# Kernel optimization log

Measured on AMD Instinct MI355X. Metric: run time of the kernel, lower is better.

Reference implementation:

```python
import jax, jax.numpy as jnp
import numpy as np

# config constants
B, S, H = 4, 2048, 1024
E = 8                 # n_routed_experts
M = 512               # moe_intermediate_size
K = 2                 # num_experts_per_tok
N_SHARED = 2
SM = M * N_SHARED     # shared expert intermediate
G = 64                # gene_size
GE_TEMP = 1.0
ALPHA = 0.001         # aux_loss_alpha
SEQ_AUX = True
NORM_TOPK = True
COS_TEMP = 0.78
CONS_ALPHA = 0.01
LEAKY_SLOPE = 0.01
EPS_COS = 1e-8


def setup_inputs() -> dict:
    key = jax.random.key(0)
    ks = jax.random.split(key, 12)
    sh = 1.0 / np.sqrt(H)
    sm = 1.0 / np.sqrt(M)
    ssm = 1.0 / np.sqrt(SM)
    sg = 1.0 / np.sqrt(G)
    return {
        "hidden_states": jax.random.normal(ks[0], (B, S, H), jnp.float32),
        "g": jax.random.normal(ks[1], (B, G), jnp.float32),
        "wt": jax.random.uniform(ks[2], (E, H), jnp.float32, -sh, sh),   # gate weight_token
        "wg": jax.random.uniform(ks[3], (E, G), jnp.float32, -sg, sg),   # gate weight_gene
        "w_gate": jax.random.uniform(ks[4], (E, H, M), jnp.float32, -sh, sh),
        "w_up": jax.random.uniform(ks[5], (E, H, M), jnp.float32, -sh, sh),
        "w_down": jax.random.uniform(ks[6], (E, M, H), jnp.float32, -sm, sm),
        "sw_gate": jax.random.uniform(ks[7], (H, SM), jnp.float32, -sh, sh),
        "sw_up": jax.random.uniform(ks[8], (H, SM), jnp.float32, -sh, sh),
        "sw_down": jax.random.uniform(ks[9], (SM, H), jnp.float32, -ssm, ssm),
    }


def _leaky(x):
    return jnp.where(x >= 0, x, LEAKY_SLOPE * x)


def _moe_forward(hidden_states, g, wt, wg, w_gate, w_up, w_down, sw_gate, sw_up, sw_down):
    b, s, h = hidden_states.shape
    x = hidden_states.reshape(-1, h)                    # [T, H], T = b*s
    T = x.shape[0]

    # ---- gate ----
    logits_h = x @ wt.T                                 # [T, E]
    logits_g = g @ wg.T                                 # [b, E]
    logits_g = jnp.repeat(logits_g, s, axis=0)          # [T, E]
    logits = (logits_h + logits_g / GE_TEMP) / (1.0 + 1.0 / GE_TEMP)
    scores = jax.nn.softmax(logits, axis=-1)            # [T, E]
    topk_w, topk_idx = jax.lax.top_k(scores, K)         # [T, K]
    if K > 1 and NORM_TOPK:
        topk_w = topk_w / (topk_w.sum(-1, keepdims=True) + 1e-20)

    # aux loss (seq_aux=True)
    onehot = jax.nn.one_hot(topk_idx.reshape(b, s * K), E, dtype=jnp.float32)  # [b, s*K, E]
    ce = onehot.sum(1) / (s * K / E)                    # [b, E]
    aux_loss = (ce * scores.reshape(b, s, E).mean(1)).sum(1).mean() * ALPHA

    # ---- routed experts: dense stacked compute, then gather ----
    gp = _leaky(jnp.einsum('th,ehm->etm', x, w_gate))   # [E, T, M]
    up = jnp.einsum('th,ehm->etm', x, w_up)
    y_all = jnp.einsum('etm,emh->eth', gp * up, w_down) # [E, T, H]
    y_sel = y_all[topk_idx, jnp.arange(T)[:, None], :]  # [T, K, H]
    y = (y_sel * topk_w[..., None]).sum(1).reshape(b, s, h)

    # ---- shared expert ----
    p = (_leaky(hidden_states @ sw_gate) * (hidden_states @ sw_up)) @ sw_down
    y = y + p

    # consistency cosine loss
    num = jnp.sum(y * p, -1)
    den = jnp.maximum(jnp.linalg.norm(y, axis=-1), EPS_COS) * jnp.maximum(jnp.linalg.norm(p, axis=-1), EPS_COS)
    closs = CONS_ALPHA * jnp.mean((num / den) / (1.0 + COS_TEMP))
    return y, aux_loss + closs


def reference(hidden_states, g, wt, wg, w_gate, w_up, w_down, sw_gate, sw_up, sw_down):
    y, _ = _moe_forward(hidden_states, g, wt, wg, w_gate, w_up, w_down, sw_gate, sw_up, sw_down)
    return y
```

## Files before the change

kernel.cpp:

```cpp
#include <hip/hip_runtime.h>
#include <stdint.h>

#define T_TOK 8192
#define H_DIM 1024
#define M_DIM 512
#define SM_DIM 1024
#define E_NUM 8
#define S_SEQ 2048
#define G_DIM 64
#define NASSIGN 16384
#define NSLOT (NASSIGN + E_NUM * 256)
#define MAX_TILES (NASSIGN / 256 + E_NUM)
#define NBLK_PLACE (NASSIGN / 256)

typedef float f32x4 __attribute__((ext_vector_type(4)));
typedef short bf16x8 __attribute__((ext_vector_type(8)));

struct TileDesc { int base; int expert; int nrows; };

#define WAITCNT_VM6 asm volatile("s_waitcnt vmcnt(6)" ::: "memory")
#define WAITCNT_VM4 asm volatile("s_waitcnt vmcnt(4)" ::: "memory")
#define WAITCNT_VM2 asm volatile("s_waitcnt vmcnt(2)" ::: "memory")
#define WAITCNT_VM0 asm volatile("s_waitcnt vmcnt(0)" ::: "memory")
#define WAITCNT_LGKM0 asm volatile("s_waitcnt lgkmcnt(0)" ::: "memory")

static __device__ __forceinline__ ushort f2b(float f) {
  union { float f; uint32_t u; } a; a.f = f;
  uint32_t r = a.u + 0x7fffu + ((a.u >> 16) & 1u);
  return (ushort)(r >> 16);
}
static __device__ __forceinline__ float b2f(ushort u) {
  union { uint32_t u; float f; } a; a.u = ((uint32_t)u) << 16;
  return a.f;
}
static __device__ __forceinline__ int imin(int a, int b) { return a < b ? a : b; }

static __device__ __forceinline__ void gll16(const void* g, void* l) {
  __builtin_amdgcn_global_load_lds(
      (const __attribute__((address_space(1))) void*)g,
      (__attribute__((address_space(3))) void*)l, 16, 0, 0);
}
static __device__ __forceinline__ int xcd_remap(int wg, int nwg) {
  return (wg & 7) * (nwg >> 3) + (wg >> 3);
}

__global__ __launch_bounds__(256) void prep_kernel(
    const float* __restrict__ x, const float* __restrict__ wt, const float* __restrict__ g,
    const float* __restrict__ wgm,
    const float* __restrict__ w_gate, const float* __restrict__ w_up,
    const float* __restrict__ w_down, const float* __restrict__ sw_gate,
    const float* __restrict__ sw_up, const float* __restrict__ sw_down,
    ushort* __restrict__ wg_t, ushort* __restrict__ wu_t,
    ushort* __restrict__ wd_t, ushort* __restrict__ swg_t,
    ushort* __restrict__ swu_t, ushort* __restrict__ swd_t,
    ushort* __restrict__ xb, int* __restrict__ tidx, float* __restrict__ tw) {
  __shared__ float tile[32][33];
  int id = blockIdx.x;
  if (id < 15360) {
    int tx = threadIdx.x & 31, ty = threadIdx.x >> 5;
    const float* src; ushort* dst; int R, C, t;
    if (id < 4096)        { src = w_gate;  dst = wg_t;  R = 1024; C = 512;  t = id; }
    else if (id < 8192)   { src = w_up;    dst = wu_t;  R = 1024; C = 512;  t = id - 4096; }
    else if (id < 12288)  { src = w_down;  dst = wd_t;  R = 512;  C = 1024; t = id - 8192; }
    else if (id < 13312)  { src = sw_gate; dst = swg_t; R = 1024; C = 1024; t = id - 12288; }
    else if (id < 14336)  { src = sw_up;   dst = swu_t; R = 1024; C = 1024; t = id - 13312; }
    else                  { src = sw_down; dst = swd_t; R = 1024; C = 1024; t = id - 14336; }
    int tc = C >> 5;
    int tpm = (R >> 5) * tc;
    int e = t / tpm, tt = t % tpm;
    int c0 = (tt % tc) * 32, r0 = (tt / tc) * 32;
    size_t bo = (size_t)e * R * C;
    src += bo; dst += bo;
#pragma unroll
    for (int i = 0; i < 4; ++i)
      tile[ty + i * 8][tx] = src[(size_t)(r0 + ty + i * 8) * C + c0 + tx];
    __syncthreads();
#pragma unroll
    for (int i = 0; i < 4; ++i)
      dst[(size_t)(c0 + ty + i * 8) * R + r0 + tx] = f2b(tile[tx][ty + i * 8]);
    return;
  }
  int id2 = id - 15360;
  int wv = threadIdx.x >> 6, lane = threadIdx.x & 63;
  int t = id2 * 4 + wv;
  const float4* xr4 = (const float4*)x + (size_t)t * 256;
  ushort4* xb4 = (ushort4*)xb + (size_t)t * 256;
  float a[E_NUM];
#pragma unroll
  for (int e = 0; e < E_NUM; ++e) a[e] = 0.f;
#pragma unroll
  for (int j = 0; j < 4; ++j) {
    float4 v = xr4[lane + 64 * j];
    ushort4 o;
    o.x = f2b(v.x); o.y = f2b(v.y); o.z = f2b(v.z); o.w = f2b(v.w);
    xb4[lane + 64 * j] = o;
#pragma unroll
    for (int e = 0; e < E_NUM; ++e) {
      float4 wv4 = ((const float4*)(wt + (size_t)e * H_DIM))[lane + 64 * j];
      a[e] += v.x * wv4.x + v.y * wv4.y + v.z * wv4.z + v.w * wv4.w;
    }
  }
#pragma unroll
  for (int e = 0; e < E_NUM; ++e)
    for (int off = 32; off; off >>= 1) a[e] += __shfl_xor(a[e], off, 64);
  float lge = 0.f;
  int b = t / S_SEQ;
  if (lane < E_NUM) {
    const float* gv = g + b * G_DIM;
    const float* wv2 = wgm + lane * G_DIM;
    for (int i = 0; i < G_DIM; ++i) lge += gv[i] * wv2[i];
  }
  float l[E_NUM];
#pragma unroll
  for (int e = 0; e < E_NUM; ++e) l[e] = 0.5f * (a[e] + __shfl(lge, e, 64));
  if (lane == 0) {
    int i1 = 0; float b1 = l[0];
#pragma unroll
    for (int e = 1; e < E_NUM; ++e) if (l[e] > b1) { b1 = l[e]; i1 = e; }
    int i2 = -1; float b2 = -1e30f;
#pragma unroll
    for (int e = 0; e < E_NUM; ++e) if (e != i1 && l[e] > b2) { b2 = l[e]; i2 = e; }
    float e2 = expf(b2 - b1);
    float inv = 1.f / (1.f + e2);
    tidx[t * 2] = i1; tidx[t * 2 + 1] = i2;
    tw[t * 2] = inv;  tw[t * 2 + 1] = e2 * inv;
  }
}

__global__ __launch_bounds__(256) void hist_kernel(const int* __restrict__ tidx,
                                                   int* __restrict__ bcount) {
  __shared__ int h[E_NUM];
  int tid = threadIdx.x;
  if (tid < E_NUM) h[tid] = 0;
  __syncthreads();
  atomicAdd(&h[tidx[blockIdx.x * 256 + tid]], 1);
  __syncthreads();
  if (tid < E_NUM) bcount[blockIdx.x * E_NUM + tid] = h[tid];
}

__global__ __launch_bounds__(64) void scan2_kernel(
    const int* __restrict__ bcount, int* __restrict__ boffs, int* __restrict__ offs,
    TileDesc* __restrict__ desc, int* __restrict__ ndesc) {
  __shared__ int cnt[E_NUM];
  __shared__ int off_s[E_NUM];
  int lane = threadIdx.x;
  if (lane < E_NUM) {
    int s = 0;
    for (int b = 0; b < NBLK_PLACE; ++b) s += bcount[b * E_NUM + lane];
    cnt[lane] = s;
  }
  __syncthreads();
  if (lane == 0) {
    int o = 0, nd = 0;
    for (int e = 0; e < E_NUM; ++e) {
      off_s[e] = o;
      offs[e] = o;
      int n = cnt[e];
      for (int tb = 0; tb < n; tb += 256) {
        desc[nd].base = o + tb; desc[nd].expert = e;
        desc[nd].nrows = imin(n - tb, 256);
        ++nd;
      }
      o += n;
    }
    offs[E_NUM] = o;
    *ndesc = nd;
  }
  __syncthreads();
  if (lane < E_NUM) {
    int run = off_s[lane];
    for (int b = 0; b < NBLK_PLACE; ++b) {
      boffs[b * E_NUM + lane] = run;
      run += bcount[b * E_NUM + lane];
    }
  }
}

__global__ __launch_bounds__(256) void place2_kernel(
    const int* __restrict__ tidx, const int* __restrict__ boffs,
    int* __restrict__ perm, int* __restrict__ slot_of) {
  __shared__ int wcnt[4][E_NUM];
  int tid = threadIdx.x, wv = tid >> 6, lane = tid & 63;
  int i = blockIdx.x * 256 + tid;
  int e = tidx[i];
  unsigned long long lower = (lane == 63) ? 0x7fffffffffffffffull : ((1ull << lane) - 1ull);
  int rank = 0;
#pragma unroll
  for (int ee = 0; ee < E_NUM; ++ee) {
    unsigned long long m = __ballot(e == ee);
    if (e == ee) rank = __popcll(m & lower);
    if (lane == 0) wcnt[wv][ee] = __popcll(m);
  }
  __syncthreads();
  int off = boffs[blockIdx.x * E_NUM + e];
  for (int w = 0; w < wv; ++w) off += wcnt[w][e];
  int pos = off + rank;
  perm[pos] = i >> 1;
  slot_of[i] = pos;
}

template <int DUAL>
static __device__ __forceinline__ void gemm_core8(
    const ushort* __restrict__ A, const ushort* __restrict__ B0,
    const ushort* __restrict__ B1, void* __restrict__ Out, int outf32,
    int Kd, int NdOut, int rowbase, int nrows, int n0,
    const int* __restrict__ perm, ushort* __restrict__ LDS) {
  int tid = threadIdx.x, wv = tid >> 6, lane = tid & 63;
  int wr = wv >> 2, wc = wv & 3;
  int lr = lane & 15, cg = lane >> 4;
  int sid = lane >> 3, dch = lane & 7;

  const ushort* apA[2][2];
  const ushort* apB[2][2];
#pragma unroll
  for (int qm = 0; qm < 2; ++qm)
#pragma unroll
    for (int k = 0; k < 2; ++k) {
      int idx = k * 64 + wv * 8 + sid;
      int gch = dch ^ (idx & 7);
      int grow = (idx >> 6) * 128 + qm * 64 + (idx & 63);
      grow = imin(grow, nrows - 1);
      int arow = perm ? perm[rowbase + grow] : rowbase + grow;
      apA[qm][k] = A + (size_t)arow * Kd + gch * 8;
    }
#pragma unroll
  for (int qn = 0; qn < 2; ++qn)
#pragma unroll
    for (int k = 0; k < 2; ++k) {
      int idx = k * 64 + wv * 8 + sid;
      int gch = dch ^ (idx & 7);
      int vrow = n0 + (idx >> 5) * 64 + qn * 32 + (idx & 31);
      const ushort* src; int brow;
      if (DUAL) {
        src = ((vrow >> 4) & 1) ? B1 : B0;
        brow = (vrow >> 5) * 16 + (vrow & 15);
      } else {
        src = B0; brow = vrow;
      }
      apB[qn][k] = src + (size_t)brow * Kd + gch * 8;
    }

  auto stgA = [&](int qm, int k, int nd) {
    gll16(apA[qm][k], LDS + nd * 16384 + qm * 8192 + (k * 512 + wv * 64) * 8);
    apA[qm][k] += 64;
  };
  auto stgB = [&](int qn, int k, int nd) {
    gll16(apB[qn][k], LDS + 32768 + nd * 16384 + qn * 8192 + (k * 512 + wv * 64) * 8);
    apB[qn][k] += 64;
  };
  auto rdA = [&](int d, int qm, int m, int kk) -> bf16x8 {
    int idx = wr * 64 + m * 16 + lr;
    int ch = (kk * 4 + cg) ^ (idx & 7);
    return *(const bf16x8*)(LDS + d * 16384 + qm * 8192 + idx * 64 + ch * 8);
  };
  auto rdB = [&](int d, int qn, int n, int kk) -> bf16x8 {
    int idx = wc * 32 + n * 16 + lr;
    int ch = (kk * 4 + cg) ^ (idx & 7);
    return *(const bf16x8*)(LDS + 32768 + d * 16384 + qn * 8192 + idx * 64 + ch * 8);
  };

  f32x4 acc[2][2][4][2];
#pragma unroll
  for (int qm = 0; qm < 2; ++qm)
#pragma unroll
    for (int qn = 0; qn < 2; ++qn)
#pragma unroll
      for (int m = 0; m < 4; ++m)
#pragma unroll
        for (int n = 0; n < 2; ++n) acc[qm][qn][m][n] = (f32x4){0.f, 0.f, 0.f, 0.f};

  int nk = Kd >> 6;
  stgA(0, 0, 0); stgA(0, 1, 0);
  stgB(0, 0, 0); stgB(0, 1, 0);
  stgB(1, 0, 0); stgB(1, 1, 0);
  stgA(1, 0, 0); stgA(1, 1, 0);
  WAITCNT_VM4;
  __builtin_amdgcn_s_barrier();

  for (int t = 0; t < nk; ++t) {
    int cur = t & 1, nxt = cur ^ 1;
    bool hn = (t + 1 < nk);
    bf16x8 a0f[4][2], a1f[4][2], b0f[2][2], b1f[2][2];

#pragma unroll
    for (int m = 0; m < 4; ++m) { a0f[m][0] = rdA(cur, 0, m, 0); a0f[m][1] = rdA(cur, 0, m, 1); }
#pragma unroll
    for (int n = 0; n < 2; ++n) { b0f[n][0] = rdB(cur, 0, n, 0); b0f[n][1] = rdB(cur, 0, n, 1); }
    if (hn) { stgA(0, 0, nxt); stgA(0, 1, nxt); WAITCNT_VM4; } else { WAITCNT_VM2; }
    WAITCNT_LGKM0;
    __builtin_amdgcn_s_barrier();
    __builtin_amdgcn_s_setprio(1);
#pragma unroll
    for (int m = 0; m < 4; ++m)
#pragma unroll
      for (int n = 0; n < 2; ++n) {
        acc[0][0][m][n] = __builtin_amdgcn_mfma_f32_16x16x32_bf16(a0f[m][0], b0f[n][0], acc[0][0][m][n], 0, 0, 0);
        acc[0][0][m][n] = __builtin_amdgcn_mfma_f32_16x16x32_bf16(a0f[m][1], b0f[n][1], acc[0][0][m][n], 0, 0, 0);
      }
    __builtin_amdgcn_s_setprio(0);

#pragma unroll
    for (int n = 0; n < 2; ++n) { b1f[n][0] = rdB(cur, 1, n, 0); b1f[n][1] = rdB(cur, 1, n, 1); }
    if (hn) { stgB(0, 0, nxt); stgB(0, 1, nxt); WAITCNT_VM4; } else { WAITCNT_VM0; }
    WAITCNT_LGKM0;
    __builtin_amdgcn_s_barrier();
    __builtin_amdgcn_s_setprio(1);
#pragma unroll
    for (int m = 0; m < 4; ++m)
#pragma unroll
      for (int n = 0; n < 2; ++n) {
        acc[0][1][m][n] = __builtin_amdgcn_mfma_f32_16x16x32_bf16(a0f[m][0], b1f[n][0], acc[0][1][m][n], 0, 0, 0);
        acc[0][1][m][n] = __builtin_amdgcn_mfma_f32_16x16x32_bf16(a0f[m][1], b1f[n][1], acc[0][1][m][n], 0, 0, 0);
      }
    __builtin_amdgcn_s_setprio(0);

#pragma unroll
    for (int m = 0; m < 4; ++m) { a1f[m][0] = rdA(cur, 1, m, 0); a1f[m][1] = rdA(cur, 1, m, 1); }
    if (hn) { stgB(1, 0, nxt); stgB(1, 1, nxt); WAITCNT_VM6; }
    WAITCNT_LGKM0;
    __builtin_amdgcn_s_barrier();
    __builtin_amdgcn_s_setprio(1);
#pragma unroll
    for (int m = 0; m < 4; ++m)
#pragma unroll
      for (int n = 0; n < 2; ++n) {
        acc[1][0][m][n] = __builtin_amdgcn_mfma_f32_16x16x32_bf16(a1f[m][0], b0f[n][0], acc[1][0][m][n], 0, 0, 0);
        acc[1][0][m][n] = __builtin_amdgcn_mfma_f32_16x16x32_bf16(a1f[m][1], b0f[n][1], acc[1][0][m][n], 0, 0, 0);
      }
    __builtin_amdgcn_s_setprio(0);

    if (hn) { stgA(1, 0, nxt); stgA(1, 1, nxt); WAITCNT_VM4; }
    WAITCNT_LGKM0;
    __builtin_amdgcn_s_barrier();
    __builtin_amdgcn_s_setprio(1);
#pragma unroll
    for (int m = 0; m < 4; ++m)
#pragma unroll
      for (int n = 0; n < 2; ++n) {
        acc[1][1][m][n] = __builtin_amdgcn_mfma_f32_16x16x32_bf16(a1f[m][0], b1f[n][0], acc[1][1][m][n], 0, 0, 0);
        acc[1][1][m][n] = __builtin_amdgcn_mfma_f32_16x16x32_bf16(a1f[m][1], b1f[n][1], acc[1][1][m][n], 0, 0, 0);
      }
    __builtin_amdgcn_s_setprio(0);
  }

#pragma unroll
  for (int qm = 0; qm < 2; ++qm)
#pragma unroll
    for (int qn = 0; qn < 2; ++qn)
#pragma unroll
      for (int m = 0; m < 4; ++m)
#pragma unroll
        for (int r = 0; r < 4; ++r) {
          int row = wr * 128 + qm * 64 + m * 16 + cg * 4 + r;
          if (row < nrows) {
            if (DUAL) {
              float gv = acc[qm][qn][m][0][r], uv = acc[qm][qn][m][1][r];
              float hv = (gv >= 0.f ? gv : 0.01f * gv) * uv;
              int col = ((n0 >> 5) + wc * 2 + qn) * 16 + lr;
              ((ushort*)Out)[(size_t)(rowbase + row) * NdOut + col] = f2b(hv);
            } else {
#pragma unroll
              for (int n = 0; n < 2; ++n) {
                int col = n0 + wc * 64 + qn * 32 + n * 16 + lr;
                size_t o = (size_t)(rowbase + row) * NdOut + col;
                if (outf32) ((float*)Out)[o] = acc[qm][qn][m][n][r];
                else ((ushort*)Out)[o] = f2b(acc[qm][qn][m][n][r]);
              }
            }
          }
        }
}

__global__ __launch_bounds__(512) void gemm_dual_all(
    const ushort* __restrict__ xb, const ushort* __restrict__ swg,
    const ushort* __restrict__ swu, ushort* __restrict__ hsh,
    const ushort* __restrict__ wg, const ushort* __restrict__ wu,
    ushort* __restrict__ h_e, const int* __restrict__ perm,
    const TileDesc* __restrict__ desc, const int* __restrict__ ndesc) {
  __shared__ ushort LDS[65536];
  int id = xcd_remap(blockIdx.x, gridDim.x);
  if (id < 256) {
    int mt = id >> 3, n0 = (id & 7) * 256;
    gemm_core8<1>(xb, swg, swu, hsh, 0, H_DIM, SM_DIM, mt * 256, 256, n0, nullptr, LDS);
  } else {
    int rid = id - 256;
    int mt = rid >> 2, n0 = (rid & 3) * 256;
    if (mt >= *ndesc) return;
    TileDesc d = desc[mt];
    size_t wo = (size_t)d.expert * M_DIM * H_DIM;
    gemm_core8<1>(xb, wg + wo, wu + wo, h_e, 0, H_DIM, M_DIM, d.base, d.nrows, n0, perm, LDS);
  }
}

__global__ __launch_bounds__(512) void gemm_down_all(
    const ushort* __restrict__ hsh, const ushort* __restrict__ swd, ushort* __restrict__ ysh,
    const ushort* __restrict__ h_e, const ushort* __restrict__ wd, ushort* __restrict__ ye,
    const TileDesc* __restrict__ desc, const int* __restrict__ ndesc) {
  __shared__ ushort LDS[65536];
  int id = xcd_remap(blockIdx.x, gridDim.x);
  if (id < 128) {
    int mt = id >> 2, n0 = (id & 3) * 256;
    gemm_core8<0>(hsh, swd, nullptr, (void*)ysh, 0, SM_DIM, H_DIM, mt * 256, 256, n0, nullptr, LDS);
  } else {
    int rid = id - 128;
    int mt = rid >> 2, n0 = (rid & 3) * 256;
    if (mt >= *ndesc) return;
    TileDesc d = desc[mt];
    gemm_core8<0>(h_e, wd + (size_t)d.expert * H_DIM * M_DIM, nullptr, (void*)ye, 0,
                  M_DIM, H_DIM, d.base, d.nrows, n0, nullptr, LDS);
  }
}

__global__ __launch_bounds__(256) void final_kernel(
    float* __restrict__ y, const ushort* __restrict__ ysh, const ushort* __restrict__ ye,
    const int* __restrict__ slot_of, const float* __restrict__ tw) {
  for (int i = blockIdx.x * 256 + threadIdx.x; i < T_TOK * H_DIM / 4; i += 2048 * 256) {
    int t = i >> 8;
    int c4 = (i & 255) * 4;
    int s0 = slot_of[t * 2], s1 = slot_of[t * 2 + 1];
    float w0 = tw[t * 2], w1 = tw[t * 2 + 1];
    ushort4 pp = *(const ushort4*)(ysh + (size_t)t * H_DIM + c4);
    ushort4 a = *(const ushort4*)(ye + (size_t)s0 * H_DIM + c4);
    ushort4 b = *(const ushort4*)(ye + (size_t)s1 * H_DIM + c4);
    float4 v;
    v.x = b2f(pp.x) + w0 * b2f(a.x) + w1 * b2f(b.x);
    v.y = b2f(pp.y) + w0 * b2f(a.y) + w1 * b2f(b.y);
    v.z = b2f(pp.z) + w0 * b2f(a.z) + w1 * b2f(b.z);
    v.w = b2f(pp.w) + w0 * b2f(a.w) + w1 * b2f(b.w);
    ((float4*)y)[i] = v;
  }
}

extern "C" void kernel_launch(void* const* d_in, const int* in_sizes, int n_in,
                              void* d_out, int out_size, void* d_ws, size_t ws_size,
                              hipStream_t stream) {
  const float* x       = (const float*)d_in[0];
  const float* g       = (const float*)d_in[1];
  const float* wt      = (const float*)d_in[2];
  const float* wg      = (const float*)d_in[3];
  const float* w_gate  = (const float*)d_in[4];
  const float* w_up    = (const float*)d_in[5];
  const float* w_down  = (const float*)d_in[6];
  const float* sw_gate = (const float*)d_in[7];
  const float* sw_up   = (const float*)d_in[8];
  const float* sw_down = (const float*)d_in[9];
  float* y = (float*)d_out;

  char* p = (char*)d_ws;
  auto alloc = [&](size_t bytes) -> char* {
    char* r = p;
    p += (bytes + 255) & ~(size_t)255;
    return r;
  };
  ushort* xb    = (ushort*)alloc((size_t)T_TOK * H_DIM * 2);
  ushort* wg_t  = (ushort*)alloc((size_t)E_NUM * M_DIM * H_DIM * 2);
  ushort* wu_t  = (ushort*)alloc((size_t)E_NUM * M_DIM * H_DIM * 2);
  ushort* wd_t  = (ushort*)alloc((size_t)E_NUM * H_DIM * M_DIM * 2);
  ushort* swg_t = (ushort*)alloc((size_t)SM_DIM * H_DIM * 2);
  ushort* swu_t = (ushort*)alloc((size_t)SM_DIM * H_DIM * 2);
  ushort* swd_t = (ushort*)alloc((size_t)H_DIM * SM_DIM * 2);
  int* tidx     = (int*)alloc(NASSIGN * 4);
  float* tw     = (float*)alloc(NASSIGN * 4);
  int* bcount   = (int*)alloc(NBLK_PLACE * E_NUM * 4);
  int* boffs    = (int*)alloc(NBLK_PLACE * E_NUM * 4);
  int* offs     = (int*)alloc((E_NUM + 1) * 4);
  int* ndesc    = (int*)alloc(4);
  int* perm     = (int*)alloc(NASSIGN * 4);
  int* slot_of  = (int*)alloc(NASSIGN * 4);
  TileDesc* desc = (TileDesc*)alloc(MAX_TILES * sizeof(TileDesc));
  ushort* h_e   = (ushort*)alloc((size_t)NSLOT * M_DIM * 2);
  ushort* hsh   = (ushort*)alloc((size_t)T_TOK * SM_DIM * 2);
  ushort* ye    = (ushort*)alloc((size_t)NSLOT * H_DIM * 2);
  ushort* ysh   = (ushort*)alloc((size_t)T_TOK * H_DIM * 2);
  (void)ws_size; (void)in_sizes; (void)n_in; (void)out_size;

  prep_kernel<<<15360 + 2048, 256, 0, stream>>>(
      x, wt, g, wg, w_gate, w_up, w_down, sw_gate, sw_up, sw_down,
      wg_t, wu_t, wd_t, swg_t, swu_t, swd_t, xb, tidx, tw);
  hist_kernel<<<NBLK_PLACE, 256, 0, stream>>>(tidx, bcount);
  scan2_kernel<<<1, 64, 0, stream>>>(bcount, boffs, offs, desc, ndesc);
  place2_kernel<<<NBLK_PLACE, 256, 0, stream>>>(tidx, boffs, perm, slot_of);

  gemm_dual_all<<<256 + MAX_TILES * 4, 512, 0, stream>>>(
      xb, swg_t, swu_t, hsh, wg_t, wu_t, h_e, perm, desc, ndesc);
  gemm_down_all<<<128 + MAX_TILES * 4, 512, 0, stream>>>(
      hsh, swd_t, ysh, h_e, wd_t, ye, desc, ndesc);

  final_kernel<<<2048, 256, 0, stream>>>(y, ysh, ye, slot_of, tw);
}
```

Baseline: 207.5 us.

## Fuse routing histogram and scan into prep and place kernels; drop redundant LDS waits

Per-chunk expert counts are now built with global atomics inside the gate/prep kernel. Each place block computes its own prefix offsets and the tile descriptors directly. This removes the separate histogram and single-block scan kernels and their launch and serialization cost, at the price of a memset, global atomics and a redundant per-block prefix loop. Separately, the GEMM main loop drops explicit lgkmcnt(0) waits before barriers and reorders the B fragment reads ahead of the A reads, leaving the compiler to place LDS waits so more latency can overlap.

New measurement: 212.8 us. +2.5%, slower.

```diff
diff --git a/kernel.cpp b/kernel.cpp
--- a/kernel.cpp
+++ b/kernel.cpp
@@ -22,7 +22,6 @@
 #define WAITCNT_VM4 asm volatile("s_waitcnt vmcnt(4)" ::: "memory")
 #define WAITCNT_VM2 asm volatile("s_waitcnt vmcnt(2)" ::: "memory")
 #define WAITCNT_VM0 asm volatile("s_waitcnt vmcnt(0)" ::: "memory")
-#define WAITCNT_LGKM0 asm volatile("s_waitcnt lgkmcnt(0)" ::: "memory")
 
 static __device__ __forceinline__ ushort f2b(float f) {
   union { float f; uint32_t u; } a; a.f = f;
@@ -53,7 +52,8 @@
     ushort* __restrict__ wg_t, ushort* __restrict__ wu_t,
     ushort* __restrict__ wd_t, ushort* __restrict__ swg_t,
     ushort* __restrict__ swu_t, ushort* __restrict__ swd_t,
-    ushort* __restrict__ xb, int* __restrict__ tidx, float* __restrict__ tw) {
+    ushort* __restrict__ xb, int* __restrict__ tidx, float* __restrict__ tw,
+    int* __restrict__ bcount) {
   __shared__ float tile[32][33];
   int id = blockIdx.x;
   if (id < 15360) {
@@ -124,37 +124,38 @@
     float inv = 1.f / (1.f + e2);
     tidx[t * 2] = i1; tidx[t * 2 + 1] = i2;
     tw[t * 2] = inv;  tw[t * 2 + 1] = e2 * inv;
-  }
-}
-
-__global__ __launch_bounds__(256) void hist_kernel(const int* __restrict__ tidx,
-                                                   int* __restrict__ bcount) {
-  __shared__ int h[E_NUM];
-  int tid = threadIdx.x;
-  if (tid < E_NUM) h[tid] = 0;
-  __syncthreads();
-  atomicAdd(&h[tidx[blockIdx.x * 256 + tid]], 1);
-  __syncthreads();
-  if (tid < E_NUM) bcount[blockIdx.x * E_NUM + tid] = h[tid];
-}
-
-__global__ __launch_bounds__(64) void scan2_kernel(
-    const int* __restrict__ bcount, int* __restrict__ boffs, int* __restrict__ offs,
+    int chunk = t >> 7;
+    atomicAdd(&bcount[chunk * E_NUM + i1], 1);
+    atomicAdd(&bcount[chunk * E_NUM + i2], 1);
+  }
+}
+
+__global__ __launch_bounds__(256) void place2_kernel(
+    const int* __restrict__ tidx, const int* __restrict__ bcount,
+    int* __restrict__ perm, int* __restrict__ slot_of,
     TileDesc* __restrict__ desc, int* __restrict__ ndesc) {
   __shared__ int cnt[E_NUM];
-  __shared__ int off_s[E_NUM];
-  int lane = threadIdx.x;
-  if (lane < E_NUM) {
-    int s = 0;
-    for (int b = 0; b < NBLK_PLACE; ++b) s += bcount[b * E_NUM + lane];
-    cnt[lane] = s;
+  __shared__ int myoff[E_NUM];
+  __shared__ int wcnt[4][E_NUM];
+  int tid = threadIdx.x, wv = tid >> 6, lane = tid & 63, blk = blockIdx.x;
+  if (tid < E_NUM) {
+    int run = 0, mine = 0;
+    for (int b = 0; b < NBLK_PLACE; ++b) {
+      if (b == blk) mine = run;
+      run += bcount[b * E_NUM + tid];
+    }
+    cnt[tid] = run;
+    myoff[tid] = mine;
   }
   __syncthreads();
-  if (lane == 0) {
+  if (tid < E_NUM) {
+    int o = 0;
+    for (int e = 0; e < tid; ++e) o += cnt[e];
+    myoff[tid] += o;
+  }
+  if (blk == 0 && tid == 32) {
     int o = 0, nd = 0;
     for (int e = 0; e < E_NUM; ++e) {
-      off_s[e] = o;
-      offs[e] = o;
       int n = cnt[e];
       for (int tb = 0; tb < n; tb += 256) {
         desc[nd].base = o + tb; desc[nd].expert = e;
@@ -163,25 +164,9 @@
       }
       o += n;
     }
-    offs[E_NUM] = o;
     *ndesc = nd;
   }
-  __syncthreads();
-  if (lane < E_NUM) {
-    int run = off_s[lane];
-    for (int b = 0; b < NBLK_PLACE; ++b) {
-      boffs[b * E_NUM + lane] = run;
-      run += bcount[b * E_NUM + lane];
-    }
-  }
-}
-
-__global__ __launch_bounds__(256) void place2_kernel(
-    const int* __restrict__ tidx, const int* __restrict__ boffs,
-    int* __restrict__ perm, int* __restrict__ slot_of) {
-  __shared__ int wcnt[4][E_NUM];
-  int tid = threadIdx.x, wv = tid >> 6, lane = tid & 63;
-  int i = blockIdx.x * 256 + tid;
+  int i = blk * 256 + tid;
   int e = tidx[i];
   unsigned long long lower = (lane == 63) ? 0x7fffffffffffffffull : ((1ull << lane) - 1ull);
   int rank = 0;
@@ -192,7 +177,7 @@
     if (lane == 0) wcnt[wv][ee] = __popcll(m);
   }
   __syncthreads();
-  int off = boffs[blockIdx.x * E_NUM + e];
+  int off = myoff[e];
   for (int w = 0; w < wv; ++w) off += wcnt[w][e];
   int pos = off + rank;
   perm[pos] = i >> 1;
@@ -283,11 +268,10 @@
     bf16x8 a0f[4][2], a1f[4][2], b0f[2][2], b1f[2][2];
 
 #pragma unroll
+    for (int n = 0; n < 2; ++n) { b0f[n][0] = rdB(cur, 0, n, 0); b0f[n][1] = rdB(cur, 0, n, 1); }
+#pragma unroll
     for (int m = 0; m < 4; ++m) { a0f[m][0] = rdA(cur, 0, m, 0); a0f[m][1] = rdA(cur, 0, m, 1); }
-#pragma unroll
-    for (int n = 0; n < 2; ++n) { b0f[n][0] = rdB(cur, 0, n, 0); b0f[n][1] = rdB(cur, 0, n, 1); }
     if (hn) { stgA(0, 0, nxt); stgA(0, 1, nxt); WAITCNT_VM4; } else { WAITCNT_VM2; }
-    WAITCNT_LGKM0;
     __builtin_amdgcn_s_barrier();
     __builtin_amdgcn_s_setprio(1);
 #pragma unroll
@@ -302,7 +286,6 @@
 #pragma unroll
     for (int n = 0; n < 2; ++n) { b1f[n][0] = rdB(cur, 1, n, 0); b1f[n][1] = rdB(cur, 1, n, 1); }
     if (hn) { stgB(0, 0, nxt); stgB(0, 1, nxt); WAITCNT_VM4; } else { WAITCNT_VM0; }
-    WAITCNT_LGKM0;
     __builtin_amdgcn_s_barrier();
     __builtin_amdgcn_s_setprio(1);
 #pragma unroll
@@ -317,7 +300,6 @@
 #pragma unroll
     for (int m = 0; m < 4; ++m) { a1f[m][0] = rdA(cur, 1, m, 0); a1f[m][1] = rdA(cur, 1, m, 1); }
     if (hn) { stgB(1, 0, nxt); stgB(1, 1, nxt); WAITCNT_VM6; }
-    WAITCNT_LGKM0;
     __builtin_amdgcn_s_barrier();
     __builtin_amdgcn_s_setprio(1);
 #pragma unroll
@@ -330,7 +312,6 @@
     __builtin_amdgcn_s_setprio(0);
 
     if (hn) { stgA(1, 0, nxt); stgA(1, 1, nxt); WAITCNT_VM4; }
-    WAITCNT_LGKM0;
     __builtin_amdgcn_s_barrier();
     __builtin_amdgcn_s_setprio(1);
 #pragma unroll
@@ -462,8 +443,6 @@
   int* tidx     = (int*)alloc(NASSIGN * 4);
   float* tw     = (float*)alloc(NASSIGN * 4);
   int* bcount   = (int*)alloc(NBLK_PLACE * E_NUM * 4);
-  int* boffs    = (int*)alloc(NBLK_PLACE * E_NUM * 4);
-  int* offs     = (int*)alloc((E_NUM + 1) * 4);
   int* ndesc    = (int*)alloc(4);
   int* perm     = (int*)alloc(NASSIGN * 4);
   int* slot_of  = (int*)alloc(NASSIGN * 4);
@@ -474,12 +453,11 @@
   ushort* ysh   = (ushort*)alloc((size_t)T_TOK * H_DIM * 2);
   (void)ws_size; (void)in_sizes; (void)n_in; (void)out_size;
 
+  hipMemsetAsync(bcount, 0, NBLK_PLACE * E_NUM * 4, stream);
   prep_kernel<<<15360 + 2048, 256, 0, stream>>>(
       x, wt, g, wg, w_gate, w_up, w_down, sw_gate, sw_up, sw_down,
-      wg_t, wu_t, wd_t, swg_t, swu_t, swd_t, xb, tidx, tw);
-  hist_kernel<<<NBLK_PLACE, 256, 0, stream>>>(tidx, bcount);
-  scan2_kernel<<<1, 64, 0, stream>>>(bcount, boffs, offs, desc, ndesc);
-  place2_kernel<<<NBLK_PLACE, 256, 0, stream>>>(tidx, boffs, perm, slot_of);
+      wg_t, wu_t, wd_t, swg_t, swu_t, swd_t, xb, tidx, tw, bcount);
+  place2_kernel<<<NBLK_PLACE, 256, 0, stream>>>(tidx, bcount, perm, slot_of, desc, ndesc);
 
   gemm_dual_all<<<256 + MAX_TILES * 4, 512, 0, stream>>>(
       xb, swg_t, swu_t, hsh, wg_t, wu_t, h_e, perm, desc, ndesc);
```
